# Performance work log

Measured on AMD Instinct MI355X. Metric: run time of the kernel, lower is better.

The kernel has to match this reference:

```python
import jax, jax.numpy as jnp
import numpy as np

NUM_HEADS = 8
NUM_LEVELS = 4
NUM_POINTS = 8
EMBED = 256
SPATIAL_SHAPES = ((92, 160), (46, 80), (23, 40), (12, 20))


def _bilinear_sample(vl, gx, gy, H, W):
    # vl: [N, d, H*W]; gx, gy: [N, Q, P], grid coords in [-1, 1]
    # matches F.grid_sample(mode='bilinear', padding_mode='zeros', align_corners=False)
    x = (gx + 1.0) * (W * 0.5) - 0.5
    y = (gy + 1.0) * (H * 0.5) - 0.5
    x0 = jnp.floor(x)
    y0 = jnp.floor(y)
    wx = x - x0
    wy = y - y0
    x0i = x0.astype(jnp.int32)
    y0i = y0.astype(jnp.int32)
    N, Q, P = gx.shape
    d = vl.shape[1]

    def gather(xi, yi):
        valid = ((xi >= 0) & (xi < W) & (yi >= 0) & (yi < H)).astype(vl.dtype)
        idx = jnp.clip(yi, 0, H - 1) * W + jnp.clip(xi, 0, W - 1)  # [N, Q, P]
        flat = jnp.broadcast_to(idx.reshape(N, 1, Q * P), (N, d, Q * P))
        got = jnp.take_along_axis(vl, flat, axis=2).reshape(N, d, Q, P)
        return got * valid[:, None]

    return (gather(x0i, y0i) * ((1 - wx) * (1 - wy))[:, None]
            + gather(x0i + 1, y0i) * (wx * (1 - wy))[:, None]
            + gather(x0i, y0i + 1) * ((1 - wx) * wy)[:, None]
            + gather(x0i + 1, y0i + 1) * (wx * wy)[:, None])


def _forward(query, value, reference_points, spatial_shapes,
             W_off, b_off, W_attn, b_attn, W_val, b_val, W_out, b_out):
    shapes = np.asarray(spatial_shapes)  # static per-level (H, W)
    bs, Q, C = query.shape
    H, Lv, P = NUM_HEADS, NUM_LEVELS, NUM_POINTS
    d = C // H
    # value projection, split into heads: [bs*H, d, Ltot]
    v = value @ W_val + b_val
    v = v.reshape(bs, -1, H, d).transpose(0, 2, 3, 1).reshape(bs * H, d, -1)
    # sampling offsets [bs, Q, H, Lv, P, 2]
    off = (query @ W_off + b_off).reshape(bs, Q, H, Lv, P, 2)
    # attention weights, softmax over Lv*P
    aw = jax.nn.softmax((query @ W_attn + b_attn).reshape(bs, Q, H, Lv * P), axis=-1)
    aw = aw.reshape(bs, Q, H, Lv, P).transpose(0, 2, 1, 3, 4).reshape(bs * H, Q, Lv, P)
    # normalize offsets by level (W, H)
    norm = jnp.asarray([[w_, h_] for h_, w_ in shapes], dtype=query.dtype)  # [Lv, 2]
    loc = reference_points[:, :, None, :, None, :] + off / norm[None, None, None, :, None, :]
    grids = (2.0 * loc - 1.0).transpose(0, 2, 1, 3, 4, 5).reshape(bs * H, Q, Lv, P, 2)
    out = jnp.zeros((bs * H, d, Q), dtype=query.dtype)
    start = 0
    for lvl in range(Lv):
        H_l, W_l = int(shapes[lvl, 0]), int(shapes[lvl, 1])
        vl = v[:, :, start:start + H_l * W_l]
        g = grids[:, :, lvl]  # [bs*H, Q, P, 2]
        s = _bilinear_sample(vl, g[..., 0], g[..., 1], H_l, W_l)  # [bs*H, d, Q, P]
        out = out + jnp.einsum('ndqp,nqp->ndq', s, aw[:, :, lvl])
        start += H_l * W_l
    out = out.reshape(bs, H, d, Q).transpose(0, 3, 1, 2).reshape(bs, Q, C)
    return out @ W_out + b_out


def setup_inputs() -> dict:
    key = jax.random.key(0)
    ks = jax.random.split(key, 9)
    bs, Q = 6, 4096  # 6 cameras x (64x64 BEV queries)
    Ltot = sum(h * w for h, w in SPATIAL_SHAPES)  # 19560
    HLP2 = NUM_HEADS * NUM_LEVELS * NUM_POINTS * 2  # 512
    HLP = NUM_HEADS * NUM_LEVELS * NUM_POINTS  # 256
    s = 0.02
    return {
        "query": jax.random.normal(ks[0], (bs, Q, EMBED), jnp.float32),
        "value": jax.random.normal(ks[1], (bs, Ltot, EMBED), jnp.float32),
        "reference_points": jax.random.uniform(ks[2], (bs, Q, NUM_LEVELS, 2), jnp.float32),
        "spatial_shapes": jnp.asarray(SPATIAL_SHAPES, jnp.int32),
        "W_off": s * jax.random.normal(ks[3], (EMBED, HLP2), jnp.float32),
        "b_off": s * jax.random.normal(ks[4], (HLP2,), jnp.float32),
        "W_attn": s * jax.random.normal(ks[5], (EMBED, HLP), jnp.float32),
        "b_attn": s * jax.random.normal(ks[6], (HLP,), jnp.float32),
        "W_val": s * jax.random.normal(ks[7], (EMBED, EMBED), jnp.float32),
        "b_val": jnp.zeros((EMBED,), jnp.float32),
        "W_out": s * jax.random.normal(ks[8], (EMBED, EMBED), jnp.float32),
        "b_out": jnp.zeros((EMBED,), jnp.float32),
    }


def reference(query, value, reference_points, spatial_shapes,
              W_off, b_off, W_attn, b_attn, W_val, b_val, W_out, b_out):
    return _forward(query, value, reference_points, spatial_shapes,
                    W_off, b_off, W_attn, b_attn, W_val, b_val, W_out, b_out)
```

## Files before the change

### kernel.cpp

```cpp
#include <hip/hip_runtime.h>
#include <hip/hip_fp16.h>
#include <stdint.h>

#define BS 6
#define NQ 4096
#define NH 8
#define EMB 256
#define LTOT 19560
#define ROWS_V 117360
#define ROWS_VP 117376
#define ROWS_Q 24576

typedef __attribute__((ext_vector_type(8))) short bf16x8;
typedef __attribute__((ext_vector_type(4))) float floatx4;
typedef __attribute__((ext_vector_type(8))) unsigned short ushort8v;

__device__ __forceinline__ ushort f2bf(float f) {
    union { float f; uint32_t i; } c; c.f = f;
    uint32_t r = c.i + 0x7FFFu + ((c.i >> 16) & 1u);
    return (ushort)(r >> 16);
}
__device__ __forceinline__ ushort f2h(float f) {
    __half h = __float2half(f);
    union { __half h; ushort u; } c; c.h = h; return c.u;
}
__device__ __forceinline__ float h2f(ushort u) {
    union { ushort u; __half h; } c; c.u = u; return __half2float(c.h);
}

__device__ __forceinline__ void gll16(const ushort* g, ushort* l) {
    __builtin_amdgcn_global_load_lds(
        (const __attribute__((address_space(1))) void*)g,
        (__attribute__((address_space(3))) void*)l, 16, 0, 0);
}

template<int L>
__device__ __forceinline__ float bcastf(float x) {
    return __int_as_float(
        __builtin_amdgcn_ds_swizzle(__float_as_int(x), 0x1C | (L << 5)));
}
template<int L>
__device__ __forceinline__ uint32_t bcastu(uint32_t x) {
    return (uint32_t)__builtin_amdgcn_ds_swizzle((int)x, 0x1C | (L << 5));
}

__device__ __forceinline__ void fmx_lo(float& acc, float w, uint32_t u) {
    asm("v_fma_mix_f32 %0, %1, %2, %0 op_sel:[0,0,0] op_sel_hi:[0,1,0]"
        : "+v"(acc) : "v"(w), "v"(u));
}
__device__ __forceinline__ void fmx_hi(float& acc, float w, uint32_t u) {
    asm("v_fma_mix_f32 %0, %1, %2, %0 op_sel:[0,1,0] op_sel_hi:[0,1,0]"
        : "+v"(acc) : "v"(w), "v"(u));
}

__global__ __launch_bounds__(256) void prep(
    const float* __restrict__ W_val, const float* __restrict__ W_off,
    const float* __restrict__ W_attn, const float* __restrict__ W_out,
    const float* __restrict__ b_off, const float* __restrict__ b_attn,
    ushort* __restrict__ Wvt, ushort* __restrict__ Wq,
    ushort* __restrict__ Wot, float* __restrict__ bcat)
{
    int id = blockIdx.x * 256 + threadIdx.x;
    if (id < 65536) {
        int n = id >> 8, k = id & 255;
        Wvt[id] = f2bf(W_val[k * 256 + n]);
        return;
    }
    id -= 65536;
    if (id < 131072) {
        int n = id >> 8, k = id & 255;
        Wq[id] = f2bf(W_off[k * 512 + n]);
        return;
    }
    id -= 131072;
    if (id < 65536) {
        int n = id >> 8, k = id & 255;
        Wq[131072 + id] = f2bf(W_attn[k * 256 + n]);
        return;
    }
    id -= 65536;
    if (id < 65536) {
        int n = id >> 8, k = id & 255;
        Wot[id] = f2bf(W_out[k * 256 + n]);
        return;
    }
    id -= 65536;
    if (id < 768) bcat[id] = (id < 512) ? b_off[id] : b_attn[id - 512];
}

__global__ __launch_bounds__(512) void vgemm(
    const float* __restrict__ A,
    const ushort* __restrict__ Bt,
    const float* __restrict__ bias,
    ushort* __restrict__ C)
{
    constexpr int K = 256, N = 256, M = ROWS_V;
    __shared__ ushort As[128 * 32];
    __shared__ ushort Bs[256 * 32];

    const int t = threadIdx.x;
    const int w = t >> 6;
    const int lane = t & 63;
    const int bm = blockIdx.x * 128;
    const int wm = (w >> 2) * 64;
    const int wn = (w & 3) * 64;

    const int arow = t >> 2;
    const int acol = (t & 3) * 8;
    const bool rowok = (bm + arow) < M;
    const float* Ap = A + (size_t)(bm + arow) * K + acol;
    ushort* Asw = &As[arow * 32 + acol];

    const int srow = lane >> 2;
    const int scol = (lane & 3) * 8;
    const ushort* Bg0 = Bt + (size_t)(w * 32 + srow) * K + scol;
    const ushort* Bg1 = Bt + (size_t)(w * 32 + 16 + srow) * K + scol;
    ushort* Bl0 = &Bs[(w * 32) * 32];
    ushort* Bl1 = &Bs[(w * 32 + 16) * 32];

    const ushort* apt = &As[(wm + (lane & 15)) * 32 + (lane >> 4) * 8];
    const ushort* bpt = &Bs[(wn + (lane & 15)) * 32 + (lane >> 4) * 8];

    floatx4 acc[4][4] = {};

    for (int kt = 0; kt < K; kt += 32) {
        float4 f0, f1;
        if (rowok) {
            f0 = *(const float4*)(Ap + kt);
            f1 = *(const float4*)(Ap + kt + 4);
        } else {
            f0 = make_float4(0.f, 0.f, 0.f, 0.f);
            f1 = f0;
        }
        __syncthreads();
        gll16(Bg0 + kt, Bl0);
        gll16(Bg1 + kt, Bl1);
        ushort8v u;
        u[0] = f2bf(f0.x); u[1] = f2bf(f0.y); u[2] = f2bf(f0.z); u[3] = f2bf(f0.w);
        u[4] = f2bf(f1.x); u[5] = f2bf(f1.y); u[6] = f2bf(f1.z); u[7] = f2bf(f1.w);
        *(ushort8v*)Asw = u;
        __syncthreads();

        bf16x8 a[4], b[4];
        #pragma unroll
        for (int i = 0; i < 4; ++i) {
            a[i] = *(const bf16x8*)(apt + i * 16 * 32);
            b[i] = *(const bf16x8*)(bpt + i * 16 * 32);
        }
        #pragma unroll
        for (int i = 0; i < 4; ++i)
            #pragma unroll
            for (int j = 0; j < 4; ++j)
                acc[i][j] = __builtin_amdgcn_mfma_f32_16x16x32_bf16(
                    a[i], b[j], acc[i][j], 0, 0, 0);
    }

    const int crow = (lane >> 4) * 4;
    const int ccol = lane & 15;
    #pragma unroll
    for (int j = 0; j < 4; ++j) {
        int gcol = wn + j * 16 + ccol;
        float bv = bias[gcol];
        #pragma unroll
        for (int i = 0; i < 4; ++i) {
            #pragma unroll
            for (int r = 0; r < 4; ++r) {
                int grow = bm + wm + i * 16 + crow + r;
                if (grow < M)
                    C[(size_t)grow * N + gcol] = f2h(acc[i][j][r] + bv);
            }
        }
    }
}

__global__ __launch_bounds__(256) void qgemm(
    const float* __restrict__ A,
    const ushort* __restrict__ Bt,
    const float* __restrict__ bias,
    ushort* __restrict__ C)
{
    constexpr int K = 256, N = 768;
    __shared__ ushort As[128 * 32];
    __shared__ ushort Bs[128 * 32];

    const int t = threadIdx.x;
    const int w = t >> 6;
    const int lane = t & 63;
    const int bm = blockIdx.x * 128;
    const int bn = blockIdx.y * 128;
    const int wm = (w >> 1) * 64;
    const int wn = (w & 1) * 64;

    const int arow = t >> 1;
    const int acol = (t & 1) * 16;
    const float* Ap = A + (size_t)(bm + arow) * K + acol;
    ushort* Asw = &As[arow * 32 + acol];

    const int srow = lane >> 2;
    const int scol = (lane & 3) * 8;
    const ushort* Bg0 = Bt + (size_t)(bn + w * 32 + srow) * K + scol;
    const ushort* Bg1 = Bt + (size_t)(bn + w * 32 + 16 + srow) * K + scol;
    ushort* Bl0 = &Bs[(w * 32) * 32];
    ushort* Bl1 = &Bs[(w * 32 + 16) * 32];

    const ushort* apt = &As[(wm + (lane & 15)) * 32 + (lane >> 4) * 8];
    const ushort* bpt = &Bs[(wn + (lane & 15)) * 32 + (lane >> 4) * 8];

    floatx4 acc[4][4] = {};

    for (int kt = 0; kt < K; kt += 32) {
        float4 f0 = *(const float4*)(Ap + kt);
        float4 f1 = *(const float4*)(Ap + kt + 4);
        float4 f2 = *(const float4*)(Ap + kt + 8);
        float4 f3 = *(const float4*)(Ap + kt + 12);
        __syncthreads();
        gll16(Bg0 + kt, Bl0);
        gll16(Bg1 + kt, Bl1);
        ushort8v u0, u1;
        u0[0] = f2bf(f0.x); u0[1] = f2bf(f0.y); u0[2] = f2bf(f0.z); u0[3] = f2bf(f0.w);
        u0[4] = f2bf(f1.x); u0[5] = f2bf(f1.y); u0[6] = f2bf(f1.z); u0[7] = f2bf(f1.w);
        u1[0] = f2bf(f2.x); u1[1] = f2bf(f2.y); u1[2] = f2bf(f2.z); u1[3] = f2bf(f2.w);
        u1[4] = f2bf(f3.x); u1[5] = f2bf(f3.y); u1[6] = f2bf(f3.z); u1[7] = f2bf(f3.w);
        *(ushort8v*)Asw = u0;
        *(ushort8v*)(Asw + 8) = u1;
        __syncthreads();

        bf16x8 a[4], b[4];
        #pragma unroll
        for (int i = 0; i < 4; ++i) {
            a[i] = *(const bf16x8*)(apt + i * 16 * 32);
            b[i] = *(const bf16x8*)(bpt + i * 16 * 32);
        }
        #pragma unroll
        for (int i = 0; i < 4; ++i)
            #pragma unroll
            for (int j = 0; j < 4; ++j)
                acc[i][j] = __builtin_amdgcn_mfma_f32_16x16x32_bf16(
                    a[i], b[j], acc[i][j], 0, 0, 0);
    }

    const int crow = (lane >> 4) * 4;
    const int ccol = lane & 15;
    #pragma unroll
    for (int j = 0; j < 4; ++j) {
        int gcol = bn + wn + j * 16 + ccol;
        float bv = bias[gcol];
        #pragma unroll
        for (int i = 0; i < 4; ++i) {
            int grow = bm + wm + i * 16 + crow;
            #pragma unroll
            for (int r = 0; r < 4; ++r)
                C[(size_t)(grow + r) * N + gcol] = f2h(acc[i][j][r] + bv);
        }
    }
}

__global__ __launch_bounds__(256) void gemm_bt(
    const ushort* __restrict__ A,
    const ushort* __restrict__ Bt,
    const float* __restrict__ bias,
    float* __restrict__ C, int M, int N)
{
    constexpr int K = 256;
    __shared__ ushort As[128 * 32];
    __shared__ ushort Bs[128 * 32];

    const int t = threadIdx.x;
    const int w = t >> 6;
    const int lane = t & 63;
    const int bm = blockIdx.x * 128;
    const int bn = blockIdx.y * 128;
    const int wm = (w >> 1) * 64;
    const int wn = (w & 1) * 64;

    floatx4 acc[4][4] = {};

    const int srow = lane >> 2;
    const int scol = (lane & 3) * 8;
    const ushort* Ag0 = A + (size_t)(bm + (w * 2 + 0) * 16 + srow) * K + scol;
    const ushort* Ag1 = A + (size_t)(bm + (w * 2 + 1) * 16 + srow) * K + scol;
    const ushort* Bg0 = Bt + (size_t)(bn + (w * 2 + 0) * 16 + srow) * K + scol;
    const ushort* Bg1 = Bt + (size_t)(bn + (w * 2 + 1) * 16 + srow) * K + scol;
    ushort* Al0 = &As[(w * 2 + 0) * 512];
    ushort* Al1 = &As[(w * 2 + 1) * 512];
    ushort* Bl0 = &Bs[(w * 2 + 0) * 512];
    ushort* Bl1 = &Bs[(w * 2 + 1) * 512];

    const ushort* apt = &As[(wm + (lane & 15)) * 32 + (lane >> 4) * 8];
    const ushort* bpt = &Bs[(wn + (lane & 15)) * 32 + (lane >> 4) * 8];

    for (int kt = 0; kt < K; kt += 32) {
        __syncthreads();
        gll16(Ag0 + kt, Al0);
        gll16(Ag1 + kt, Al1);
        gll16(Bg0 + kt, Bl0);
        gll16(Bg1 + kt, Bl1);
        __syncthreads();

        bf16x8 a[4], b[4];
        #pragma unroll
        for (int i = 0; i < 4; ++i) {
            a[i] = *(const bf16x8*)(apt + i * 16 * 32);
            b[i] = *(const bf16x8*)(bpt + i * 16 * 32);
        }
        #pragma unroll
        for (int i = 0; i < 4; ++i)
            #pragma unroll
            for (int j = 0; j < 4; ++j)
                acc[i][j] = __builtin_amdgcn_mfma_f32_16x16x32_bf16(
                    a[i], b[j], acc[i][j], 0, 0, 0);
    }

    const int crow = (lane >> 4) * 4;
    const int ccol = lane & 15;
    #pragma unroll
    for (int j = 0; j < 4; ++j) {
        int gcol = bn + wn + j * 16 + ccol;
        float bv = bias[gcol];
        #pragma unroll
        for (int i = 0; i < 4; ++i) {
            #pragma unroll
            for (int r = 0; r < 4; ++r) {
                int grow = bm + wm + i * 16 + crow + r;
                if (grow < M)
                    C[(size_t)grow * N + gcol] = acc[i][j][r] + bv;
            }
        }
    }
}

__global__ __launch_bounds__(256) void sampler4(
    const ushort* __restrict__ v,
    const ushort* __restrict__ qp,
    const float* __restrict__ ref,
    ushort* __restrict__ agg)
{
    __shared__ char ballast[49152];
    if (blockIdx.x > 0x7FFFFFF0u) {
        ballast[threadIdx.x] = (char)threadIdx.x;
        agg[0] = (ushort)ballast[(threadIdx.x * 37) & 4095];
    }

    const int tid = threadIdx.x;
    const int g = blockIdx.x * 64 + (tid >> 2);
    const int st = tid & 3;
    const int h = g & 7;
    const int bq = g >> 3;
    const int b = blockIdx.x >> 9;

    const int Wl = 160 >> st;
    const int Hl = (st == 3) ? 12 : (92 >> st);
    const int Sl = (st == 0) ? 0 : (st == 1) ? 14720 : (st == 2) ? 18400 : 19320;

    const ushort* qrow = qp + (size_t)bq * 768;

    float px[8], py[8];
    {
        ushort8v uo0 = *(const ushort8v*)(qrow + h * 64 + st * 16);
        ushort8v uo1 = *(const ushort8v*)(qrow + h * 64 + st * 16 + 8);
        float2 rf = *(const float2*)(ref + (size_t)bq * 8 + st * 2);
        const float fW = (float)Wl, fH = (float)Hl;
        #pragma unroll
        for (int i = 0; i < 4; ++i) {
            px[i]     = fmaf(rf.x, fW, h2f(uo0[2 * i]))     - 0.5f;
            py[i]     = fmaf(rf.y, fH, h2f(uo0[2 * i + 1])) - 0.5f;
            px[i + 4] = fmaf(rf.x, fW, h2f(uo1[2 * i]))     - 0.5f;
            py[i + 4] = fmaf(rf.y, fH, h2f(uo1[2 * i + 1])) - 0.5f;
        }
    }

    float a8[8];
    {
        ushort8v ul = *(const ushort8v*)(qrow + 512 + h * 32 + st * 8);
        #pragma unroll
        for (int i = 0; i < 8; ++i) a8[i] = h2f(ul[i]);
        float m = a8[0];
        #pragma unroll
        for (int i = 1; i < 8; ++i) m = fmaxf(m, a8[i]);
        m = fmaxf(m, __shfl_xor(m, 1, 4));
        m = fmaxf(m, __shfl_xor(m, 2, 4));
        float s = 0.f;
        #pragma unroll
        for (int i = 0; i < 8; ++i) { a8[i] = __expf(a8[i] - m); s += a8[i]; }
        s += __shfl_xor(s, 1, 4);
        s += __shfl_xor(s, 2, 4);
        float inv = 1.f / s;
        #pragma unroll
        for (int i = 0; i < 8; ++i) a8[i] *= inv;
    }

    const char* vb = (const char*)(v + (size_t)b * (LTOT * EMB));
    const uint32_t coffB = (uint32_t)(h * 64 + st * 16);

    float acc[8] = {0.f, 0.f, 0.f, 0.f, 0.f, 0.f, 0.f, 0.f};

    #pragma unroll
    for (int idx = 0; idx < 8; ++idx) {
        float px_ = px[idx], py_ = py[idx];
        float x0f = floorf(px_), y0f = floorf(py_);
        float wx = px_ - x0f, wy = py_ - y0f;
        int x0 = (int)x0f, y0 = (int)y0f;
        int x1 = x0 + 1, y1 = y0 + 1;
        float vx0 = ((uint32_t)x0 < (uint32_t)Wl) ? 1.f : 0.f;
        float vx1 = ((uint32_t)x1 < (uint32_t)Wl) ? 1.f : 0.f;
        float vy0 = ((uint32_t)y0 < (uint32_t)Hl) ? 1.f : 0.f;
        float vy1 = ((uint32_t)y1 < (uint32_t)Hl) ? 1.f : 0.f;
        int cx0 = min(max(x0, 0), Wl - 1);
        int cx1 = min(max(x1, 0), Wl - 1);
        int cy0 = min(max(y0, 0), Hl - 1);
        int cy1 = min(max(y1, 0), Hl - 1);
        float aw = a8[idx];
        float omx = 1.f - wx, omy = 1.f - wy;
        float omya = omy * aw, wya = wy * aw;
        float w00 = omx * omya * (vx0 * vy0);
        float w10 = wx  * omya * (vx1 * vy0);
        float w01 = omx * wya  * (vx0 * vy1);
        float w11 = wx  * wya  * (vx1 * vy1);
        int r0 = Sl + cy0 * Wl;
        int r1 = Sl + cy1 * Wl;
        uint32_t e00 = (uint32_t)(r0 + cx0) << 9;
        uint32_t e10 = (uint32_t)(r0 + cx1) << 9;
        uint32_t e01 = (uint32_t)(r1 + cx0) << 9;
        uint32_t e11 = (uint32_t)(r1 + cx1) << 9;

        #define ACCMIX(w_, c_) \
            fmx_lo(acc[0], w_, c_.x); fmx_hi(acc[1], w_, c_.x); \
            fmx_lo(acc[2], w_, c_.y); fmx_hi(acc[3], w_, c_.y); \
            fmx_lo(acc[4], w_, c_.z); fmx_hi(acc[5], w_, c_.z); \
            fmx_lo(acc[6], w_, c_.w); fmx_hi(acc[7], w_, c_.w);
        #define DO_LEVEL(L) { \
            float W00 = bcastf<L>(w00), W10 = bcastf<L>(w10); \
            float W01 = bcastf<L>(w01), W11 = bcastf<L>(w11); \
            uint32_t E00 = bcastu<L>(e00), E10 = bcastu<L>(e10); \
            uint32_t E01 = bcastu<L>(e01), E11 = bcastu<L>(e11); \
            uint4 c00 = *(const uint4*)(vb + (E00 + coffB)); \
            uint4 c10 = *(const uint4*)(vb + (E10 + coffB)); \
            uint4 c01 = *(const uint4*)(vb + (E01 + coffB)); \
            uint4 c11 = *(const uint4*)(vb + (E11 + coffB)); \
            ACCMIX(W00, c00); ACCMIX(W10, c10); \
            ACCMIX(W01, c01); ACCMIX(W11, c11); }
        DO_LEVEL(0)
        DO_LEVEL(1)
        DO_LEVEL(2)
        DO_LEVEL(3)
        #undef DO_LEVEL
        #undef ACCMIX
    }

    ushort8v r;
    #pragma unroll
    for (int i = 0; i < 8; ++i) r[i] = f2bf(acc[i]);
    *(ushort8v*)(agg + (size_t)bq * 256 + h * 32 + st * 8) = r;
}

extern "C" void kernel_launch(void* const* d_in, const int* in_sizes, int n_in,
                              void* d_out, int out_size, void* d_ws, size_t ws_size,
                              hipStream_t stream) {
    const float* query  = (const float*)d_in[0];
    const float* value  = (const float*)d_in[1];
    const float* refpts = (const float*)d_in[2];
    const float* W_off  = (const float*)d_in[4];
    const float* b_off  = (const float*)d_in[5];
    const float* W_attn = (const float*)d_in[6];
    const float* b_attn = (const float*)d_in[7];
    const float* W_val  = (const float*)d_in[8];
    const float* b_val  = (const float*)d_in[9];
    const float* W_out  = (const float*)d_in[10];
    const float* b_out  = (const float*)d_in[11];
    float* out = (float*)d_out;

    char* ws = (char*)d_ws;
    ushort* v_bf   = (ushort*)(ws);
    ushort* qp     = (ushort*)(ws + 72679424ull);
    ushort* agg_bf = (ushort*)(ws + 148176896ull);
    ushort* Wvt    = (ushort*)(ws + 160759808ull);
    ushort* Wq     = (ushort*)(ws + 160890880ull);
    ushort* Wot    = (ushort*)(ws + 161284096ull);
    float*  bcat   = (float*) (ws + 161415168ull);

    prep<<<1283, 256, 0, stream>>>(W_val, W_off, W_attn, W_out,
                                   b_off, b_attn, Wvt, Wq, Wot, bcat);

    vgemm<<<ROWS_VP / 128, 512, 0, stream>>>(value, Wvt, b_val, v_bf);

    qgemm<<<dim3(ROWS_Q / 128, 6), 256, 0, stream>>>(query, Wq, bcat, qp);

    sampler4<<<(ROWS_Q * NH) / 64, 256, 0, stream>>>(
        v_bf, qp, refpts, agg_bf);

    gemm_bt<<<dim3(ROWS_Q / 128, 2), 256, 0, stream>>>(
        agg_bf, Wot, b_out, out, ROWS_Q, 256);
}
```

Before: 423.2 us.

## Merge value and query projection GEMMs into one launch; remap sampler block order

The separate value-projection and query-projection GEMM kernels are combined into a single 512-thread kernel that branches on block index. The query part is retiled to 128x128 tiles across 8 waves, with each wave owning 32x64. This removes one launch and lets the smaller query GEMM fill idle compute units alongside the value GEMM's tail. The sampler also permutes its block index so that consecutively scheduled blocks map to different batches/XCDs, aiming for better cache locality per die. The cost is a smaller per-wave tile for the query path and a larger block size there.

```diff
diff --git a/kernel.cpp b/kernel.cpp
--- a/kernel.cpp
+++ b/kernel.cpp
@@ -10,6 +10,8 @@
 #define ROWS_V 117360
 #define ROWS_VP 117376
 #define ROWS_Q 24576
+#define VBLK 917
+#define QBLK 1152
 
 typedef __attribute__((ext_vector_type(8))) short bf16x8;
 typedef __attribute__((ext_vector_type(4))) float floatx4;
@@ -88,169 +90,159 @@
     if (id < 768) bcat[id] = (id < 512) ? b_off[id] : b_attn[id - 512];
 }
 
-__global__ __launch_bounds__(512) void vgemm(
-    const float* __restrict__ A,
-    const ushort* __restrict__ Bt,
-    const float* __restrict__ bias,
-    ushort* __restrict__ C)
+__global__ __launch_bounds__(512) void front(
+    const float* __restrict__ value,
+    const float* __restrict__ query,
+    const ushort* __restrict__ Wvt,
+    const ushort* __restrict__ Wq,
+    const float* __restrict__ b_val,
+    const float* __restrict__ bcat,
+    ushort* __restrict__ v_out,
+    ushort* __restrict__ qp_out)
 {
-    constexpr int K = 256, N = 256, M = ROWS_V;
+    constexpr int K = 256;
     __shared__ ushort As[128 * 32];
     __shared__ ushort Bs[256 * 32];
 
     const int t = threadIdx.x;
     const int w = t >> 6;
     const int lane = t & 63;
-    const int bm = blockIdx.x * 128;
-    const int wm = (w >> 2) * 64;
-    const int wn = (w & 3) * 64;
-
-    const int arow = t >> 2;
-    const int acol = (t & 3) * 8;
-    const bool rowok = (bm + arow) < M;
-    const float* Ap = A + (size_t)(bm + arow) * K + acol;
-    ushort* Asw = &As[arow * 32 + acol];
-
-    const int srow = lane >> 2;
-    const int scol = (lane & 3) * 8;
-    const ushort* Bg0 = Bt + (size_t)(w * 32 + srow) * K + scol;
-    const ushort* Bg1 = Bt + (size_t)(w * 32 + 16 + srow) * K + scol;
-    ushort* Bl0 = &Bs[(w * 32) * 32];
-    ushort* Bl1 = &Bs[(w * 32 + 16) * 32];
-
-    const ushort* apt = &As[(wm + (lane & 15)) * 32 + (lane >> 4) * 8];
-    const ushort* bpt = &Bs[(wn + (lane & 15)) * 32 + (lane >> 4) * 8];
-
-    floatx4 acc[4][4] = {};
-
-    for (int kt = 0; kt < K; kt += 32) {
-        float4 f0, f1;
-        if (rowok) {
-            f0 = *(const float4*)(Ap + kt);
-            f1 = *(const float4*)(Ap + kt + 4);
-        } else {
-            f0 = make_float4(0.f, 0.f, 0.f, 0.f);
-            f1 = f0;
-        }
-        __syncthreads();
-        gll16(Bg0 + kt, Bl0);
-        gll16(Bg1 + kt, Bl1);
-        ushort8v u;
-        u[0] = f2bf(f0.x); u[1] = f2bf(f0.y); u[2] = f2bf(f0.z); u[3] = f2bf(f0.w);
-        u[4] = f2bf(f1.x); u[5] = f2bf(f1.y); u[6] = f2bf(f1.z); u[7] = f2bf(f1.w);
-        *(ushort8v*)Asw = u;
-        __syncthreads();
-
-        bf16x8 a[4], b[4];
-        #pragma unroll
-        for (int i = 0; i < 4; ++i) {
-            a[i] = *(const bf16x8*)(apt + i * 16 * 32);
-            b[i] = *(const bf16x8*)(bpt + i * 16 * 32);
-        }
-        #pragma unroll
-        for (int i = 0; i < 4; ++i)
+    const int bid = blockIdx.x;
+
+    if (bid < VBLK) {
+        constexpr int N = 256, M = ROWS_V;
+        const int bm = bid * 128;
+        const int wm = (w >> 2) * 64;
+        const int wn = (w & 3) * 64;
+
+        const int arow = t >> 2;
+        const int acol = (t & 3) * 8;
+        const bool rowok = (bm + arow) < M;
+        const float* Ap = value + (size_t)(bm + arow) * K + acol;
+        ushort* Asw = &As[arow * 32 + acol];
+
+        const int srow = lane >> 2;
+        const int scol = (lane & 3) * 8;
+        const ushort* Bg0 = Wvt + (size_t)(w * 32 + srow) * K + scol;
+        const ushort* Bg1 = Wvt + (size_t)(w * 32 + 16 + srow) * K + scol;
+        ushort* Bl0 = &Bs[(w * 32) * 32];
+        ushort* Bl1 = &Bs[(w * 32 + 16) * 32];
+
+        const ushort* apt = &As[(wm + (lane & 15)) * 32 + (lane >> 4) * 8];
+        const ushort* bpt = &Bs[(wn + (lane & 15)) * 32 + (lane >> 4) * 8];
+
+        floatx4 acc[4][4] = {};
+
+        for (int kt = 0; kt < K; kt += 32) {
+            float4 f0, f1;
+            if (rowok) {
+                f0 = *(const float4*)(Ap + kt);
+                f1 = *(const float4*)(Ap + kt + 4);
+            } else {
+                f0 = make_float4(0.f, 0.f, 0.f, 0.f);
+                f1 = f0;
+            }
+            __syncthreads();
+            gll16(Bg0 + kt, Bl0);
+            gll16(Bg1 + kt, Bl1);
+            ushort8v u;
+            u[0] = f2bf(f0.x); u[1] = f2bf(f0.y); u[2] = f2bf(f0.z); u[3] = f2bf(f0.w);
+            u[4] = f2bf(f1.x); u[5] = f2bf(f1.y); u[6] = f2bf(f1.z); u[7] = f2bf(f1.w);
+            *(ushort8v*)Asw = u;
+            __syncthreads();
+
+            bf16x8 a[4], b[4];
+            #pragma unroll
+            for (int i = 0; i < 4; ++i) {
+                a[i] = *(const bf16x8*)(apt + i * 16 * 32);
+                b[i] = *(const bf16x8*)(bpt + i * 16 * 32);
+            }
+            #pragma unroll
+            for (int i = 0; i < 4; ++i)
+                #pragma unroll
+                for (int j = 0; j < 4; ++j)
+                    acc[i][j] = __builtin_amdgcn_mfma_f32_16x16x32_bf16(
+                        a[i], b[j], acc[i][j], 0, 0, 0);
+        }
+
+        const int crow = (lane >> 4) * 4;
+        const int ccol = lane & 15;
+        #pragma unroll
+        for (int j = 0; j < 4; ++j) {
+            int gcol = wn + j * 16 + ccol;
+            float bv = b_val[gcol];
+            #pragma unroll
+            for (int i = 0; i < 4; ++i) {
+                #pragma unroll
+                for (int r = 0; r < 4; ++r) {
+                    int grow = bm + wm + i * 16 + crow + r;
+                    if (grow < M)
+                        v_out[(size_t)grow * N + gcol] = f2h(acc[i][j][r] + bv);
+                }
+            }
+        }
+    } else {
+        constexpr int N = 768;
+        const int qbid = bid - VBLK;
+        const int bm = (qbid % 192) * 128;
+        const int bn = (qbid / 192) * 128;
+        const int wm = (w >> 1) * 32;
+        const int wn = (w & 1) * 64;
+
+        const int arow = t >> 2;
+        const int acol = (t & 3) * 8;
+        const float* Ap = query + (size_t)(bm + arow) * K + acol;
+        ushort* Asw = &As[arow * 32 + acol];
+
+        const int srow = lane >> 2;
+        const int scol = (lane & 3) * 8;
+        const ushort* Bg0 = Wq + (size_t)(bn + w * 16 + srow) * K + scol;
+        ushort* Bl0 = &Bs[(w * 16) * 32];
+
+        const ushort* apt = &As[(wm + (lane & 15)) * 32 + (lane >> 4) * 8];
+        const ushort* bpt = &Bs[(wn + (lane & 15)) * 32 + (lane >> 4) * 8];
+
+        floatx4 acc[2][4] = {};
+
+        for (int kt = 0; kt < K; kt += 32) {
+            float4 f0 = *(const float4*)(Ap + kt);
+            float4 f1 = *(const float4*)(Ap + kt + 4);
+            __syncthreads();
+            gll16(Bg0 + kt, Bl0);
+            ushort8v u;
+            u[0] = f2bf(f0.x); u[1] = f2bf(f0.y); u[2] = f2bf(f0.z); u[3] = f2bf(f0.w);
+            u[4] = f2bf(f1.x); u[5] = f2bf(f1.y); u[6] = f2bf(f1.z); u[7] = f2bf(f1.w);
+            *(ushort8v*)Asw = u;
+            __syncthreads();
+
+            bf16x8 a[2], b[4];
+            #pragma unroll
+            for (int i = 0; i < 2; ++i)
+                a[i] = *(const bf16x8*)(apt + i * 16 * 32);
             #pragma unroll
             for (int j = 0; j < 4; ++j)
-                acc[i][j] = __builtin_amdgcn_mfma_f32_16x16x32_bf16(
-                    a[i], b[j], acc[i][j], 0, 0, 0);
-    }
-
-    const int crow = (lane >> 4) * 4;
-    const int ccol = lane & 15;
-    #pragma unroll
-    for (int j = 0; j < 4; ++j) {
-        int gcol = wn + j * 16 + ccol;
-        float bv = bias[gcol];
-        #pragma unroll
-        for (int i = 0; i < 4; ++i) {
-            #pragma unroll
-            for (int r = 0; r < 4; ++r) {
-                int grow = bm + wm + i * 16 + crow + r;
-                if (grow < M)
-                    C[(size_t)grow * N + gcol] = f2h(acc[i][j][r] + bv);
+                b[j] = *(const bf16x8*)(bpt + j * 16 * 32);
+            #pragma unroll
+            for (int i = 0; i < 2; ++i)
+                #pragma unroll
+                for (int j = 0; j < 4; ++j)
+                    acc[i][j] = __builtin_amdgcn_mfma_f32_16x16x32_bf16(
+                        a[i], b[j], acc[i][j], 0, 0, 0);
+        }
+
+        const int crow = (lane >> 4) * 4;
+        const int ccol = lane & 15;
+        #pragma unroll
+        for (int j = 0; j < 4; ++j) {
+            int gcol = bn + wn + j * 16 + ccol;
+            float bv = bcat[gcol];
+            #pragma unroll
+            for (int i = 0; i < 2; ++i) {
+                int grow = bm + wm + i * 16 + crow;
+                #pragma unroll
+                for (int r = 0; r < 4; ++r)
+                    qp_out[(size_t)(grow + r) * N + gcol] = f2h(acc[i][j][r] + bv);
             }
-        }
-    }
-}
-
-__global__ __launch_bounds__(256) void qgemm(
-    const float* __restrict__ A,
-    const ushort* __restrict__ Bt,
-    const float* __restrict__ bias,
-    ushort* __restrict__ C)
-{
-    constexpr int K = 256, N = 768;
-    __shared__ ushort As[128 * 32];
-    __shared__ ushort Bs[128 * 32];
-
-    const int t = threadIdx.x;
-    const int w = t >> 6;
-    const int lane = t & 63;
-    const int bm = blockIdx.x * 128;
-    const int bn = blockIdx.y * 128;
-    const int wm = (w >> 1) * 64;
-    const int wn = (w & 1) * 64;
-
-    const int arow = t >> 1;
-    const int acol = (t & 1) * 16;
-    const float* Ap = A + (size_t)(bm + arow) * K + acol;
-    ushort* Asw = &As[arow * 32 + acol];
-
-    const int srow = lane >> 2;
-    const int scol = (lane & 3) * 8;
-    const ushort* Bg0 = Bt + (size_t)(bn + w * 32 + srow) * K + scol;
-    const ushort* Bg1 = Bt + (size_t)(bn + w * 32 + 16 + srow) * K + scol;
-    ushort* Bl0 = &Bs[(w * 32) * 32];
-    ushort* Bl1 = &Bs[(w * 32 + 16) * 32];
-
-    const ushort* apt = &As[(wm + (lane & 15)) * 32 + (lane >> 4) * 8];
-    const ushort* bpt = &Bs[(wn + (lane & 15)) * 32 + (lane >> 4) * 8];
-
-    floatx4 acc[4][4] = {};
-
-    for (int kt = 0; kt < K; kt += 32) {
-        float4 f0 = *(const float4*)(Ap + kt);
-        float4 f1 = *(const float4*)(Ap + kt + 4);
-        float4 f2 = *(const float4*)(Ap + kt + 8);
-        float4 f3 = *(const float4*)(Ap + kt + 12);
-        __syncthreads();
-        gll16(Bg0 + kt, Bl0);
-        gll16(Bg1 + kt, Bl1);
-        ushort8v u0, u1;
-        u0[0] = f2bf(f0.x); u0[1] = f2bf(f0.y); u0[2] = f2bf(f0.z); u0[3] = f2bf(f0.w);
-        u0[4] = f2bf(f1.x); u0[5] = f2bf(f1.y); u0[6] = f2bf(f1.z); u0[7] = f2bf(f1.w);
-        u1[0] = f2bf(f2.x); u1[1] = f2bf(f2.y); u1[2] = f2bf(f2.z); u1[3] = f2bf(f2.w);
-        u1[4] = f2bf(f3.x); u1[5] = f2bf(f3.y); u1[6] = f2bf(f3.z); u1[7] = f2bf(f3.w);
-        *(ushort8v*)Asw = u0;
-        *(ushort8v*)(Asw + 8) = u1;
-        __syncthreads();
-
-        bf16x8 a[4], b[4];
-        #pragma unroll
-        for (int i = 0; i < 4; ++i) {
-            a[i] = *(const bf16x8*)(apt + i * 16 * 32);
-            b[i] = *(const bf16x8*)(bpt + i * 16 * 32);
-        }
-        #pragma unroll
-        for (int i = 0; i < 4; ++i)
-            #pragma unroll
-            for (int j = 0; j < 4; ++j)
-                acc[i][j] = __builtin_amdgcn_mfma_f32_16x16x32_bf16(
-                    a[i], b[j], acc[i][j], 0, 0, 0);
-    }
-
-    const int crow = (lane >> 4) * 4;
-    const int ccol = lane & 15;
-    #pragma unroll
-    for (int j = 0; j < 4; ++j) {
-        int gcol = bn + wn + j * 16 + ccol;
-        float bv = bias[gcol];
-        #pragma unroll
-        for (int i = 0; i < 4; ++i) {
-            int grow = bm + wm + i * 16 + crow;
-            #pragma unroll
-            for (int r = 0; r < 4; ++r)
-                C[(size_t)(grow + r) * N + gcol] = f2h(acc[i][j][r] + bv);
         }
     }
 }
@@ -341,12 +333,14 @@
         agg[0] = (ushort)ballast[(threadIdx.x * 37) & 4095];
     }
 
+    const int bid = (blockIdx.x & 7) * 384 + (blockIdx.x >> 3);
+
     const int tid = threadIdx.x;
-    const int g = blockIdx.x * 64 + (tid >> 2);
+    const int g = bid * 64 + (tid >> 2);
     const int st = tid & 3;
     const int h = g & 7;
     const int bq = g >> 3;
-    const int b = blockIdx.x >> 9;
+    const int b = bid >> 9;
 
     const int Wl = 160 >> st;
     const int Hl = (st == 3) ? 12 : (92 >> st);
@@ -481,9 +475,8 @@
     prep<<<1283, 256, 0, stream>>>(W_val, W_off, W_attn, W_out,
                                    b_off, b_attn, Wvt, Wq, Wot, bcat);
 
-    vgemm<<<ROWS_VP / 128, 512, 0, stream>>>(value, Wvt, b_val, v_bf);
-
-    qgemm<<<dim3(ROWS_Q / 128, 6), 256, 0, stream>>>(query, Wq, bcat, qp);
+    front<<<VBLK + QBLK, 512, 0, stream>>>(
+        value, query, Wvt, Wq, b_val, bcat, v_bf, qp);
 
     sampler4<<<(ROWS_Q * NH) / 64, 256, 0, stream>>>(
         v_bf, qp, refpts, agg_bf);
```

Result: faster. 404.8 us (-4.3%).
